# Kernel tuning notes

Measured on AMD Instinct MI355X. Metric: run time of the kernel, lower is better.

The kernel has to match this reference:

```python
import jax, jax.numpy as jnp
import numpy as np

WEIGHTS = {'seg': 1.0, 'grid': 0.5, 'baseline': 0.8, 'theta': 0.3, 'signal': 2.0}
IGNORE = 255


def _bce(p, t):
    # torch BCELoss: clamps log terms at -100
    lp = jnp.maximum(jnp.log(jnp.clip(p, 1e-12, 1.0)), -100.0)
    l1p = jnp.maximum(jnp.log(jnp.clip(1.0 - p, 1e-12, 1.0)), -100.0)
    return -(t * lp + (1.0 - t) * l1p).mean()


def _ce_ignore(logits, target):
    # logits (B,C,H,W), target (B,H,W) int; mean over target != 255
    logp = jax.nn.log_softmax(logits, axis=1)
    valid = target != IGNORE
    t_safe = jnp.where(valid, target, 0)
    nll = -jnp.take_along_axis(logp, t_safe[:, None].astype(jnp.int32), axis=1)[:, 0]
    return (nll * valid).sum() / jnp.maximum(valid.sum(), 1)


def _dice(logits, target, num_classes):
    p = jax.nn.softmax(logits, axis=1)                      # (B,C,H,W)
    oh = jax.nn.one_hot(target, num_classes, dtype=p.dtype) # (B,H,W,C)
    oh = jnp.transpose(oh, (0, 3, 1, 2))
    inter = (p * oh).sum(axis=(2, 3))
    union = p.sum(axis=(2, 3)) + oh.sum(axis=(2, 3))
    dice = (2.0 * inter + 1e-07) / (union + 1e-07)
    return 1.0 - dice.mean()


def _resize_bilinear_ac(x, out_h, out_w):
    # align_corners=True bilinear, x: (B,C,H,W)
    B, C, H, Wd = x.shape
    ys = jnp.linspace(0.0, H - 1.0, out_h)
    xs = jnp.linspace(0.0, Wd - 1.0, out_w)
    y0 = jnp.floor(ys).astype(jnp.int32); y1 = jnp.minimum(y0 + 1, H - 1); wy = (ys - y0).astype(x.dtype)
    x0 = jnp.floor(xs).astype(jnp.int32); x1 = jnp.minimum(x0 + 1, Wd - 1); wx = (xs - x0).astype(x.dtype)
    rows = x[:, :, y0, :] * (1 - wy)[None, None, :, None] + x[:, :, y1, :] * wy[None, None, :, None]
    out = rows[:, :, :, x0] * (1 - wx) + rows[:, :, :, x1] * wx
    return out


def _normalize_signal_masked(sig, mask):
    # sig, mask: (B,12,T); per-lead min/max normalize on valid region
    mf = mask.astype(sig.dtype)
    cnt = mf.sum(-1, keepdims=True)
    mn = jnp.min(jnp.where(mask, sig, jnp.inf), -1, keepdims=True)
    mx = jnp.max(jnp.where(mask, sig, -jnp.inf), -1, keepdims=True)
    rng = mx - mn
    ok = (cnt >= 2) & (rng >= 1e-06)
    mn_s = jnp.where(ok, mn, 0.0)
    rng_s = jnp.where(ok, rng, 1.0)
    norm = (2.0 * (sig - mn_s) / (rng_s + 1e-08) - 1.0) * mf
    return jnp.where(ok, norm, 0.0)


def _masked_mae(pred, target, mask):
    mf = mask.astype(pred.dtype)
    return (jnp.abs(pred - target) * mf).sum() / (mf.sum() + 1e-07)


def _masked_pearson(pred, target, mask):
    mf = mask.astype(pred.dtype)
    cnt = mf.sum(-1)                                   # (B,12)
    cs = jnp.maximum(cnt, 1.0)
    pm = (pred * mf).sum(-1) / cs
    tm = (target * mf).sum(-1) / cs
    pc = (pred - pm[..., None]) * mf
    tc = (target - tm[..., None]) * mf
    num = (pc * tc).sum(-1)
    ps = jnp.sqrt((pc ** 2).sum(-1) + 1e-06)
    ts = jnp.sqrt((tc ** 2).sum(-1) + 1e-06)
    corr = jnp.clip(num / (ps * ts + 1e-06), -1.0, 1.0)
    valid = (cnt >= 10).astype(pred.dtype)
    n_valid = valid.sum()
    avg = (corr * valid).sum() / jnp.maximum(n_valid, 1.0)
    return jnp.where(n_valid > 0, 1.0 - avg, 1.0)


def setup_inputs() -> dict:
    key = jax.random.key(0)
    ks = jax.random.split(key, 11)
    B, H, Wd, T = 8, 512, 512, 5000
    return {
        'wave_seg_pred': jax.random.normal(ks[0], (B, 13, H, Wd), jnp.float32),
        'wave_seg_target': jax.random.randint(ks[1], (B, H, Wd), 0, 13, jnp.int32),
        'grid_pred': jax.random.uniform(ks[2], (B, 1, H, Wd), jnp.float32),
        'grid_target': jax.random.uniform(ks[3], (B, 1, H, Wd), jnp.float32),
        'baseline_pred': jax.random.uniform(ks[4], (B, 12, H // 16, Wd // 16), jnp.float32),
        'baseline_target': jax.random.uniform(ks[5], (B, 12, H, Wd), jnp.float32),
        'theta_pred': jax.random.normal(ks[6], (B, 2, 3), jnp.float32),
        'theta_gt': jax.random.normal(ks[7], (B, 2, 3), jnp.float32),
        'signal_pred': jax.random.normal(ks[8], (B, 12, T), jnp.float32),
        'gt_signal': jax.random.normal(ks[9], (B, T, 12), jnp.float32),
        'signal_mask': jax.random.randint(ks[10], (B, T, 12), 0, 2, jnp.int32).astype(bool),
    }


def reference(wave_seg_pred, wave_seg_target, grid_pred, grid_target,
              baseline_pred, baseline_target, theta_pred, theta_gt,
              signal_pred, gt_signal, signal_mask):
    # seg
    seg = (_ce_ignore(wave_seg_pred, wave_seg_target)
           + _dice(wave_seg_pred, wave_seg_target, 13)) * WEIGHTS['seg']
    # grid
    inter = (grid_pred * grid_target).sum()
    union = grid_pred.sum() + grid_target.sum()
    grid = (_bce(grid_pred, grid_target)
            + (1.0 - (2.0 * inter + 1e-07) / (union + 1e-07))) * WEIGHTS['grid']
    # baseline
    Hp, Wp = baseline_pred.shape[2], baseline_pred.shape[3]
    bt = _resize_bilinear_ac(baseline_target, Hp, Wp)
    baseline = _bce(baseline_pred, bt) * WEIGHTS['baseline']
    # theta
    theta = jnp.abs(theta_pred - theta_gt).mean() * WEIGHTS['theta']
    # signal
    sig_t = jnp.swapaxes(gt_signal, 1, 2)     # (B,12,T)
    m = jnp.swapaxes(signal_mask, 1, 2)       # (B,12,T)
    pn = _normalize_signal_masked(signal_pred, m)
    tn = _normalize_signal_masked(sig_t, m)
    signal = (_masked_mae(pn, tn, m) + _masked_pearson(pn, tn, m)) * WEIGHTS['signal']
    total = seg + grid + baseline + theta + signal
    return jnp.stack([seg, grid, baseline, theta, signal, total])
```

## Files before the change

### kernel.cpp

```cpp
#include <hip/hip_runtime.h>
#include <math.h>

#define WS_SEG_NLL    0
#define WS_SEG_VALID  8
#define WS_INTER      16
#define WS_PSUM       120
#define WS_OHCNT      224
#define WS_GRID_BCE   328
#define WS_GRID_INTER 329
#define WS_GRID_PSUM  330
#define WS_GRID_TSUM  331
#define WS_BASE_BCE   332
#define WS_SIG_ABS    333
#define WS_SIG_CNT    334
#define WS_SIG_CORR   335
#define WS_SIG_NV     336
#define WS_FLOATS     338

__device__ inline float wave_sum(float v) {
    #pragma unroll
    for (int o = 32; o > 0; o >>= 1) v += __shfl_down(v, o, 64);
    return v;
}

template <int OP>
__device__ inline float blk_red(float v, float* sb) {
    #pragma unroll
    for (int o = 32; o > 0; o >>= 1) {
        float u = __shfl_down(v, o, 64);
        v = (OP == 0) ? (v + u) : ((OP == 1) ? fminf(v, u) : fmaxf(v, u));
    }
    __syncthreads();
    if ((threadIdx.x & 63) == 0) sb[threadIdx.x >> 6] = v;
    __syncthreads();
    const int nw = blockDim.x >> 6;
    float r = sb[0];
    for (int w = 1; w < nw; w++) {
        float u = sb[w];
        r = (OP == 0) ? (r + u) : ((OP == 1) ? fminf(r, u) : fmaxf(r, u));
    }
    return r;
}

__global__ __launch_bounds__(256) void seg_kernel(const float4* __restrict__ pred4,
                                                  const int4* __restrict__ tgt4,
                                                  float* __restrict__ ws) {
    const int b = blockIdx.y;
    const int HW  = 512 * 512;
    const int HW4 = HW / 4;
    const float4* predb = pred4 + (size_t)b * 13 * HW4;
    const int4* tgtb = tgt4 + (size_t)b * HW4;

    float psum[13], inter[13], cnt13[13];
    #pragma unroll
    for (int c = 0; c < 13; c++) { psum[c] = 0.f; inter[c] = 0.f; cnt13[c] = 0.f; }
    float nll = 0.f, nval = 0.f;

    const int stride = gridDim.x * blockDim.x;
    for (int i = blockIdx.x * blockDim.x + threadIdx.x; i < HW4; i += stride) {
        float4 x4[13];
        #pragma unroll
        for (int c = 0; c < 13; c++) x4[c] = predb[(size_t)c * HW4 + i];
        const int4 t4 = tgtb[i];
        const int ta[4] = {t4.x, t4.y, t4.z, t4.w};
        #pragma unroll
        for (int k = 0; k < 4; k++) {
            float x[13];
            #pragma unroll
            for (int c = 0; c < 13; c++)
                x[c] = (k == 0) ? x4[c].x : (k == 1) ? x4[c].y : (k == 2) ? x4[c].z : x4[c].w;
            const int t = ta[k];
            float m = x[0];
            #pragma unroll
            for (int c = 1; c < 13; c++) m = fmaxf(m, x[c]);
            float xt = x[0];
            #pragma unroll
            for (int c = 1; c < 13; c++) xt = (c == t) ? x[c] : xt;
            float se = 0.f;
            #pragma unroll
            for (int c = 0; c < 13; c++) { x[c] = __expf(x[c] - m); se += x[c]; }
            const float inv = 1.0f / se;
            #pragma unroll
            for (int c = 0; c < 13; c++) {
                const float p = x[c] * inv;
                psum[c] += p;
                const bool sel = (c == t);
                inter[c] += sel ? p : 0.f;
                cnt13[c] += sel ? 1.f : 0.f;
            }
            const bool valid = (t != 255);
            nll  += valid ? (m + __logf(se) - xt) : 0.f;
            nval += valid ? 1.f : 0.f;
        }
    }

    __shared__ float sred[41];
    if (threadIdx.x < 41) sred[threadIdx.x] = 0.f;
    __syncthreads();
    const bool lane0 = (threadIdx.x & 63) == 0;
    #pragma unroll
    for (int c = 0; c < 13; c++) {
        float a = wave_sum(psum[c]);  if (lane0) atomicAdd(&sred[c], a);
        float d = wave_sum(inter[c]); if (lane0) atomicAdd(&sred[13 + c], d);
        float e = wave_sum(cnt13[c]); if (lane0) atomicAdd(&sred[26 + c], e);
    }
    { float a = wave_sum(nll);  if (lane0) atomicAdd(&sred[39], a); }
    { float a = wave_sum(nval); if (lane0) atomicAdd(&sred[40], a); }
    __syncthreads();
    if (threadIdx.x < 13) {
        atomicAdd(&ws[WS_PSUM  + b * 13 + threadIdx.x], sred[threadIdx.x]);
        atomicAdd(&ws[WS_INTER + b * 13 + threadIdx.x], sred[13 + threadIdx.x]);
        atomicAdd(&ws[WS_OHCNT + b * 13 + threadIdx.x], sred[26 + threadIdx.x]);
    }
    if (threadIdx.x == 64) atomicAdd(&ws[WS_SEG_NLL + b],   sred[39]);
    if (threadIdx.x == 65) atomicAdd(&ws[WS_SEG_VALID + b], sred[40]);
}

__global__ __launch_bounds__(256) void grid_kernel(const float4* __restrict__ gp,
                                                   const float4* __restrict__ gt,
                                                   float* __restrict__ ws) {
    const int N4 = 2097152 / 4;
    float bce = 0.f, inter = 0.f, ps = 0.f, ts = 0.f;
    const int stride = gridDim.x * blockDim.x;
    for (int i = blockIdx.x * blockDim.x + threadIdx.x; i < N4; i += stride) {
        const float4 p4 = gp[i];
        const float4 t4 = gt[i];
        const float pa[4] = {p4.x, p4.y, p4.z, p4.w};
        const float ta[4] = {t4.x, t4.y, t4.z, t4.w};
        #pragma unroll
        for (int k = 0; k < 4; k++) {
            const float p = pa[k], t = ta[k];
            const float pc  = fminf(fmaxf(p, 1e-12f), 1.0f);
            const float qc  = fminf(fmaxf(1.f - p, 1e-12f), 1.0f);
            const float lp  = fmaxf(__logf(pc), -100.f);
            const float l1p = fmaxf(__logf(qc), -100.f);
            bce  -= t * lp + (1.f - t) * l1p;
            inter += p * t;
            ps += p;
            ts += t;
        }
    }
    __shared__ float s4[4];
    if (threadIdx.x < 4) s4[threadIdx.x] = 0.f;
    __syncthreads();
    const bool lane0 = (threadIdx.x & 63) == 0;
    { float a = wave_sum(bce);   if (lane0) atomicAdd(&s4[0], a); }
    { float a = wave_sum(inter); if (lane0) atomicAdd(&s4[1], a); }
    { float a = wave_sum(ps);    if (lane0) atomicAdd(&s4[2], a); }
    { float a = wave_sum(ts);    if (lane0) atomicAdd(&s4[3], a); }
    __syncthreads();
    if (threadIdx.x == 0) {
        atomicAdd(&ws[WS_GRID_BCE],   s4[0]);
        atomicAdd(&ws[WS_GRID_INTER], s4[1]);
        atomicAdd(&ws[WS_GRID_PSUM],  s4[2]);
        atomicAdd(&ws[WS_GRID_TSUM],  s4[3]);
    }
}

__global__ __launch_bounds__(256) void baseline_kernel(const float* __restrict__ bp,
                                                       const float* __restrict__ bt,
                                                       float* __restrict__ ws) {
    const int idx = blockIdx.x * blockDim.x + threadIdx.x;
    float bce = 0.f;
    {
        const int w  = idx & 31;
        const int h  = (idx >> 5) & 31;
        const int bc = idx >> 10;
        const float* img = bt + (size_t)bc * 262144;
        const float step = 511.0f / 31.0f;
        const float yy = h * step, xx = w * step;
        int y0 = (int)floorf(yy); int y1 = min(y0 + 1, 511); const float wy = yy - y0;
        int x0 = (int)floorf(xx); int x1 = min(x0 + 1, 511); const float wx = xx - x0;
        const float v00 = img[y0 * 512 + x0], v01 = img[y0 * 512 + x1];
        const float v10 = img[y1 * 512 + x0], v11 = img[y1 * 512 + x1];
        const float r0 = v00 * (1.f - wy) + v10 * wy;
        const float r1 = v01 * (1.f - wy) + v11 * wy;
        const float t  = r0 * (1.f - wx) + r1 * wx;
        const float p  = bp[idx];
        const float pc  = fminf(fmaxf(p, 1e-12f), 1.0f);
        const float qc  = fminf(fmaxf(1.f - p, 1e-12f), 1.0f);
        const float lp  = fmaxf(__logf(pc), -100.f);
        const float l1p = fmaxf(__logf(qc), -100.f);
        bce = -(t * lp + (1.f - t) * l1p);
    }
    __shared__ float sb[4];
    const float s = blk_red<0>(bce, sb);
    if (threadIdx.x == 0) atomicAdd(&ws[WS_BASE_BCE], s);
}

__global__ __launch_bounds__(256) void signal_kernel(const float* __restrict__ sp,
                                                     const float* __restrict__ st,
                                                     const void* __restrict__ mp,
                                                     float* __restrict__ ws) {
    const int T = 5000;
    const int bl = blockIdx.x;
    const int b = bl / 12, l = bl % 12;
    const float* ps = sp + (size_t)(b * 12 + l) * T;
    const float* ts_base = st + (size_t)b * T * 12 + l;
    const int* mi = (const int*)mp;
    const unsigned char* mb = (const unsigned char*)mp;
    const size_t mbase = (size_t)b * T * 12 + l;

    __shared__ float sb[4];
    __shared__ int s_flag;

    if (threadIdx.x == 0) s_flag = 0;
    __syncthreads();
    int f = 0;
    for (int i = threadIdx.x; i < 3072; i += blockDim.x)
        if ((i & 3) && mb[i]) f = 1;
    if (__any(f) && (threadIdx.x & 63) == 0) atomicOr(&s_flag, 1);
    __syncthreads();
    const bool m32 = (s_flag == 0);

    float cnt = 0.f;
    float mnp = __builtin_inff(), mxp = -__builtin_inff();
    float mnt = __builtin_inff(), mxt = -__builtin_inff();
    for (int t = threadIdx.x; t < T; t += blockDim.x) {
        const bool m = m32 ? (mi[mbase + (size_t)t * 12] != 0)
                           : (mb[mbase + (size_t)t * 12] != 0);
        const float p  = ps[t];
        const float tv = ts_base[(size_t)t * 12];
        if (m) {
            cnt += 1.f;
            mnp = fminf(mnp, p);  mxp = fmaxf(mxp, p);
            mnt = fminf(mnt, tv); mxt = fmaxf(mxt, tv);
        }
    }
    cnt = blk_red<0>(cnt, sb);
    mnp = blk_red<1>(mnp, sb); mxp = blk_red<2>(mxp, sb);
    mnt = blk_red<1>(mnt, sb); mxt = blk_red<2>(mxt, sb);

    const float rngp = mxp - mnp, rngt = mxt - mnt;
    const bool okp = (cnt >= 2.f) && (rngp >= 1e-6f);
    const bool okt = (cnt >= 2.f) && (rngt >= 1e-6f);
    const float mnp_s = okp ? mnp : 0.f, rp = okp ? rngp : 1.f;
    const float mnt_s = okt ? mnt : 0.f, rt = okt ? rngt : 1.f;
    const float invp = 2.f / (rp + 1e-8f), invt = 2.f / (rt + 1e-8f);

    float S_p = 0.f, S_t = 0.f, S_pt = 0.f, S_pp = 0.f, S_tt = 0.f, S_abs = 0.f;
    for (int t = threadIdx.x; t < T; t += blockDim.x) {
        const bool m = m32 ? (mi[mbase + (size_t)t * 12] != 0)
                           : (mb[mbase + (size_t)t * 12] != 0);
        const float p  = ps[t];
        const float tv = ts_base[(size_t)t * 12];
        const float pn = (m && okp) ? ((p  - mnp_s) * invp - 1.f) : 0.f;
        const float tn = (m && okt) ? ((tv - mnt_s) * invt - 1.f) : 0.f;
        S_p += pn; S_t += tn;
        S_pt += pn * tn; S_pp += pn * pn; S_tt += tn * tn;
        S_abs += m ? fabsf(pn - tn) : 0.f;
    }
    S_p  = blk_red<0>(S_p, sb);
    S_t  = blk_red<0>(S_t, sb);
    S_pt = blk_red<0>(S_pt, sb);
    S_pp = blk_red<0>(S_pp, sb);
    S_tt = blk_red<0>(S_tt, sb);
    S_abs = blk_red<0>(S_abs, sb);

    if (threadIdx.x == 0) {
        const float cs = fmaxf(cnt, 1.f);
        const float pm = S_p / cs, tm = S_t / cs;
        const float num = S_pt - pm * S_t - tm * S_p + pm * tm * cnt;
        const float psd = sqrtf(fmaxf(S_pp - 2.f * pm * S_p + pm * pm * cnt, 0.f) + 1e-6f);
        const float tsd = sqrtf(fmaxf(S_tt - 2.f * tm * S_t + tm * tm * cnt, 0.f) + 1e-6f);
        float corr = num / (psd * tsd + 1e-6f);
        corr = fminf(fmaxf(corr, -1.f), 1.f);
        const float valid = (cnt >= 10.f) ? 1.f : 0.f;
        atomicAdd(&ws[WS_SIG_ABS],  S_abs);
        atomicAdd(&ws[WS_SIG_CNT],  cnt);
        atomicAdd(&ws[WS_SIG_CORR], corr * valid);
        atomicAdd(&ws[WS_SIG_NV],   valid);
    }
}

__global__ __launch_bounds__(128) void finalize_kernel(const float* __restrict__ tp,
                                                       const float* __restrict__ tg,
                                                       const float* __restrict__ ws,
                                                       float* __restrict__ out) {
    __shared__ float s_d, s_nll, s_nv, s_th;
    if (threadIdx.x == 0) { s_d = 0.f; s_nll = 0.f; s_nv = 0.f; s_th = 0.f; }
    __syncthreads();
    const int t = threadIdx.x;
    float d = 0.f, nll = 0.f, nv = 0.f, th = 0.f;
    if (t < 104) {
        const float it = ws[WS_INTER + t], p = ws[WS_PSUM + t], oh = ws[WS_OHCNT + t];
        d = (2.f * it + 1e-7f) / (p + oh + 1e-7f);
    }
    if (t < 8) { nll = ws[WS_SEG_NLL + t]; nv = ws[WS_SEG_VALID + t]; }
    if (t < 48) th = fabsf(tp[t] - tg[t]);
    d = wave_sum(d); nll = wave_sum(nll); nv = wave_sum(nv); th = wave_sum(th);
    if ((t & 63) == 0) {
        atomicAdd(&s_d, d); atomicAdd(&s_nll, nll);
        atomicAdd(&s_nv, nv); atomicAdd(&s_th, th);
    }
    __syncthreads();
    if (t == 0) {
        const float ce = s_nll / fmaxf(s_nv, 1.f);
        const float seg = (ce + (1.f - s_d / 104.f)) * 1.0f;
        const float bce_g = ws[WS_GRID_BCE] / 2097152.f;
        const float gd = 1.f - (2.f * ws[WS_GRID_INTER] + 1e-7f) /
                               (ws[WS_GRID_PSUM] + ws[WS_GRID_TSUM] + 1e-7f);
        const float grid = (bce_g + gd) * 0.5f;
        const float base = (ws[WS_BASE_BCE] / 98304.f) * 0.8f;
        const float theta = (s_th / 48.f) * 0.3f;
        const float mae = ws[WS_SIG_ABS] / (ws[WS_SIG_CNT] + 1e-7f);
        const float nvs = ws[WS_SIG_NV];
        const float pear = (nvs > 0.f) ? (1.f - ws[WS_SIG_CORR] / fmaxf(nvs, 1.f)) : 1.f;
        const float sig = (mae + pear) * 2.0f;
        const float total = seg + grid + base + theta + sig;
        out[0] = seg; out[1] = grid; out[2] = base; out[3] = theta; out[4] = sig;
        out[5] = total;
    }
}

extern "C" void kernel_launch(void* const* d_in, const int* in_sizes, int n_in,
                              void* d_out, int out_size, void* d_ws, size_t ws_size,
                              hipStream_t stream) {
    const float* seg_pred  = (const float*)d_in[0];
    const int*   seg_tgt   = (const int*)d_in[1];
    const float* grid_pred = (const float*)d_in[2];
    const float* grid_tgt  = (const float*)d_in[3];
    const float* base_pred = (const float*)d_in[4];
    const float* base_tgt  = (const float*)d_in[5];
    const float* theta_p   = (const float*)d_in[6];
    const float* theta_g   = (const float*)d_in[7];
    const float* sig_p     = (const float*)d_in[8];
    const float* sig_t     = (const float*)d_in[9];
    const void*  maskp     = d_in[10];
    float* ws  = (float*)d_ws;
    float* out = (float*)d_out;

    hipMemsetAsync(d_ws, 0, WS_FLOATS * sizeof(float), stream);
    seg_kernel<<<dim3(128, 8), 256, 0, stream>>>((const float4*)seg_pred,
                                                 (const int4*)seg_tgt, ws);
    grid_kernel<<<128, 256, 0, stream>>>((const float4*)grid_pred, (const float4*)grid_tgt, ws);
    baseline_kernel<<<384, 256, 0, stream>>>(base_pred, base_tgt, ws);
    signal_kernel<<<96, 256, 0, stream>>>(sig_p, sig_t, maskp, ws);
    finalize_kernel<<<1, 128, 0, stream>>>(theta_p, theta_g, ws, out);
}
```

Baseline: 328.4 us.

## Merge loss kernels into one launch and split signal into two phases

Combines the seg, grid, baseline and signal-stats work into a single kernel dispatched by block index. The signal kernel is split into a stats phase and a second phase that also does the finalize step, using a last-block counter. Seg work is spread over many more blocks, with float2 loads, ballot-based counts and shared atomics for the intersection term. The intent is fewer launches and better occupancy on the large seg tensor, at the cost of more scattered shared atomics and an extra workspace round-trip for the signal statistics.

Result: faster. 304.8 us (-7.2%).

```diff
diff --git a/kernel.cpp b/kernel.cpp
--- a/kernel.cpp
+++ b/kernel.cpp
@@ -15,7 +15,16 @@
 #define WS_SIG_CNT    334
 #define WS_SIG_CORR   335
 #define WS_SIG_NV     336
-#define WS_FLOATS     338
+#define WS_MASK_FLAG  337
+#define WS_DONE       338
+#define WS_SIGSTATS   340
+#define WS_FLOATS     820
+
+#define SEG_NB   2048
+#define GRID_NB  256
+#define BASE_NB  384
+#define SIGA_NB  96
+#define TOTAL_NB (SEG_NB + GRID_NB + BASE_NB + SIGA_NB)
 
 __device__ inline float wave_sum(float v) {
     #pragma unroll
@@ -42,34 +51,46 @@
     return r;
 }
 
-__global__ __launch_bounds__(256) void seg_kernel(const float4* __restrict__ pred4,
-                                                  const int4* __restrict__ tgt4,
-                                                  float* __restrict__ ws) {
-    const int b = blockIdx.y;
-    const int HW  = 512 * 512;
-    const int HW4 = HW / 4;
-    const float4* predb = pred4 + (size_t)b * 13 * HW4;
-    const int4* tgtb = tgt4 + (size_t)b * HW4;
-
-    float psum[13], inter[13], cnt13[13];
-    #pragma unroll
-    for (int c = 0; c < 13; c++) { psum[c] = 0.f; inter[c] = 0.f; cnt13[c] = 0.f; }
-    float nll = 0.f, nval = 0.f;
-
-    const int stride = gridDim.x * blockDim.x;
-    for (int i = blockIdx.x * blockDim.x + threadIdx.x; i < HW4; i += stride) {
-        float4 x4[13];
+__device__ void seg_part(int sb_idx, const float2* __restrict__ pred2,
+                         const int2* __restrict__ tgt2, float* __restrict__ ws) {
+    const int b  = sb_idx >> 8;
+    const int xb = sb_idx & 255;
+    const int HW2 = 131072;
+    const float2* predb = pred2 + (size_t)b * 13 * HW2;
+    const int2*   tgtb  = tgt2 + (size_t)b * HW2;
+
+    __shared__ float s_inter[13];
+    __shared__ float s_psum[13];
+    __shared__ int   s_cnt[13];
+    __shared__ float s_nll;
+    __shared__ int   s_nval;
+    if (threadIdx.x < 13) { s_inter[threadIdx.x] = 0.f; s_psum[threadIdx.x] = 0.f; s_cnt[threadIdx.x] = 0; }
+    if (threadIdx.x == 13) s_nll = 0.f;
+    if (threadIdx.x == 14) s_nval = 0;
+    __syncthreads();
+
+    float psum[13];
+    #pragma unroll
+    for (int c = 0; c < 13; c++) psum[c] = 0.f;
+    int cnt[13];
+    #pragma unroll
+    for (int c = 0; c < 13; c++) cnt[c] = 0;
+    float nll = 0.f;
+    int nval = 0;
+
+    #pragma unroll
+    for (int it = 0; it < 2; it++) {
+        const int j = xb * 256 + threadIdx.x + it * 65536;
+        float2 x2[13];
         #pragma unroll
-        for (int c = 0; c < 13; c++) x4[c] = predb[(size_t)c * HW4 + i];
-        const int4 t4 = tgtb[i];
-        const int ta[4] = {t4.x, t4.y, t4.z, t4.w};
+        for (int c = 0; c < 13; c++) x2[c] = predb[c * HW2 + j];
+        const int2 t2 = tgtb[j];
         #pragma unroll
-        for (int k = 0; k < 4; k++) {
+        for (int k = 0; k < 2; k++) {
+            const int t = (k == 0) ? t2.x : t2.y;
             float x[13];
             #pragma unroll
-            for (int c = 0; c < 13; c++)
-                x[c] = (k == 0) ? x4[c].x : (k == 1) ? x4[c].y : (k == 2) ? x4[c].z : x4[c].w;
-            const int t = ta[k];
+            for (int c = 0; c < 13; c++) x[c] = (k == 0) ? x2[c].x : x2[c].y;
             float m = x[0];
             #pragma unroll
             for (int c = 1; c < 13; c++) m = fmaxf(m, x[c]);
@@ -79,50 +100,49 @@
             float se = 0.f;
             #pragma unroll
             for (int c = 0; c < 13; c++) { x[c] = __expf(x[c] - m); se += x[c]; }
-            const float inv = 1.0f / se;
-            #pragma unroll
-            for (int c = 0; c < 13; c++) {
-                const float p = x[c] * inv;
-                psum[c] += p;
-                const bool sel = (c == t);
-                inter[c] += sel ? p : 0.f;
-                cnt13[c] += sel ? 1.f : 0.f;
+            const float inv = __builtin_amdgcn_rcpf(se);
+            #pragma unroll
+            for (int c = 0; c < 13; c++) psum[c] += x[c] * inv;
+            #pragma unroll
+            for (int c = 0; c < 13; c++) cnt[c] += __popcll(__ballot(t == c));
+            nval += __popcll(__ballot(t != 255));
+            const bool valid = (t != 255);
+            if ((unsigned)t < 13u) {
+                const float pt = __expf(xt - m) * inv;
+                atomicAdd(&s_inter[t], pt);
             }
-            const bool valid = (t != 255);
-            nll  += valid ? (m + __logf(se) - xt) : 0.f;
-            nval += valid ? 1.f : 0.f;
+            nll += valid ? (m + __logf(se) - xt) : 0.f;
         }
     }
 
-    __shared__ float sred[41];
-    if (threadIdx.x < 41) sred[threadIdx.x] = 0.f;
-    __syncthreads();
     const bool lane0 = (threadIdx.x & 63) == 0;
     #pragma unroll
     for (int c = 0; c < 13; c++) {
-        float a = wave_sum(psum[c]);  if (lane0) atomicAdd(&sred[c], a);
-        float d = wave_sum(inter[c]); if (lane0) atomicAdd(&sred[13 + c], d);
-        float e = wave_sum(cnt13[c]); if (lane0) atomicAdd(&sred[26 + c], e);
-    }
-    { float a = wave_sum(nll);  if (lane0) atomicAdd(&sred[39], a); }
-    { float a = wave_sum(nval); if (lane0) atomicAdd(&sred[40], a); }
+        float a = wave_sum(psum[c]);
+        if (lane0) atomicAdd(&s_psum[c], a);
+    }
+    { float a = wave_sum(nll); if (lane0) atomicAdd(&s_nll, a); }
+    if (lane0) {
+        #pragma unroll
+        for (int c = 0; c < 13; c++) atomicAdd(&s_cnt[c], cnt[c]);
+        atomicAdd(&s_nval, nval);
+    }
     __syncthreads();
     if (threadIdx.x < 13) {
-        atomicAdd(&ws[WS_PSUM  + b * 13 + threadIdx.x], sred[threadIdx.x]);
-        atomicAdd(&ws[WS_INTER + b * 13 + threadIdx.x], sred[13 + threadIdx.x]);
-        atomicAdd(&ws[WS_OHCNT + b * 13 + threadIdx.x], sred[26 + threadIdx.x]);
-    }
-    if (threadIdx.x == 64) atomicAdd(&ws[WS_SEG_NLL + b],   sred[39]);
-    if (threadIdx.x == 65) atomicAdd(&ws[WS_SEG_VALID + b], sred[40]);
-}
-
-__global__ __launch_bounds__(256) void grid_kernel(const float4* __restrict__ gp,
-                                                   const float4* __restrict__ gt,
-                                                   float* __restrict__ ws) {
+        atomicAdd(&ws[WS_PSUM  + b * 13 + threadIdx.x], s_psum[threadIdx.x]);
+        atomicAdd(&ws[WS_INTER + b * 13 + threadIdx.x], s_inter[threadIdx.x]);
+        atomicAdd(&ws[WS_OHCNT + b * 13 + threadIdx.x], (float)s_cnt[threadIdx.x]);
+    }
+    if (threadIdx.x == 64) atomicAdd(&ws[WS_SEG_NLL + b],   s_nll);
+    if (threadIdx.x == 65) atomicAdd(&ws[WS_SEG_VALID + b], (float)s_nval);
+}
+
+__device__ void grid_part(int gb, const float4* __restrict__ gp,
+                          const float4* __restrict__ gt, float* __restrict__ ws) {
     const int N4 = 2097152 / 4;
     float bce = 0.f, inter = 0.f, ps = 0.f, ts = 0.f;
-    const int stride = gridDim.x * blockDim.x;
-    for (int i = blockIdx.x * blockDim.x + threadIdx.x; i < N4; i += stride) {
+    const int stride = GRID_NB * 256;
+    for (int i = gb * 256 + threadIdx.x; i < N4; i += stride) {
         const float4 p4 = gp[i];
         const float4 t4 = gt[i];
         const float pa[4] = {p4.x, p4.y, p4.z, p4.w};
@@ -157,44 +177,39 @@
     }
 }
 
-__global__ __launch_bounds__(256) void baseline_kernel(const float* __restrict__ bp,
-                                                       const float* __restrict__ bt,
-                                                       float* __restrict__ ws) {
-    const int idx = blockIdx.x * blockDim.x + threadIdx.x;
-    float bce = 0.f;
-    {
-        const int w  = idx & 31;
-        const int h  = (idx >> 5) & 31;
-        const int bc = idx >> 10;
-        const float* img = bt + (size_t)bc * 262144;
-        const float step = 511.0f / 31.0f;
-        const float yy = h * step, xx = w * step;
-        int y0 = (int)floorf(yy); int y1 = min(y0 + 1, 511); const float wy = yy - y0;
-        int x0 = (int)floorf(xx); int x1 = min(x0 + 1, 511); const float wx = xx - x0;
-        const float v00 = img[y0 * 512 + x0], v01 = img[y0 * 512 + x1];
-        const float v10 = img[y1 * 512 + x0], v11 = img[y1 * 512 + x1];
-        const float r0 = v00 * (1.f - wy) + v10 * wy;
-        const float r1 = v01 * (1.f - wy) + v11 * wy;
-        const float t  = r0 * (1.f - wx) + r1 * wx;
-        const float p  = bp[idx];
-        const float pc  = fminf(fmaxf(p, 1e-12f), 1.0f);
-        const float qc  = fminf(fmaxf(1.f - p, 1e-12f), 1.0f);
-        const float lp  = fmaxf(__logf(pc), -100.f);
-        const float l1p = fmaxf(__logf(qc), -100.f);
-        bce = -(t * lp + (1.f - t) * l1p);
-    }
+__device__ void base_part(int bb, const float* __restrict__ bp,
+                          const float* __restrict__ bt, float* __restrict__ ws) {
+    const int idx = bb * 256 + threadIdx.x;
+    const int w  = idx & 31;
+    const int h  = (idx >> 5) & 31;
+    const int bc = idx >> 10;
+    const float* img = bt + (size_t)bc * 262144;
+    const float step = 511.0f / 31.0f;
+    const float yy = h * step, xx = w * step;
+    int y0 = (int)floorf(yy); int y1 = min(y0 + 1, 511); const float wy = yy - y0;
+    int x0 = (int)floorf(xx); int x1 = min(x0 + 1, 511); const float wx = xx - x0;
+    const float v00 = img[y0 * 512 + x0], v01 = img[y0 * 512 + x1];
+    const float v10 = img[y1 * 512 + x0], v11 = img[y1 * 512 + x1];
+    const float r0 = v00 * (1.f - wy) + v10 * wy;
+    const float r1 = v01 * (1.f - wy) + v11 * wy;
+    const float t  = r0 * (1.f - wx) + r1 * wx;
+    const float p  = bp[idx];
+    const float pc  = fminf(fmaxf(p, 1e-12f), 1.0f);
+    const float qc  = fminf(fmaxf(1.f - p, 1e-12f), 1.0f);
+    const float lp  = fmaxf(__logf(pc), -100.f);
+    const float l1p = fmaxf(__logf(qc), -100.f);
+    const float bce = -(t * lp + (1.f - t) * l1p);
+
     __shared__ float sb[4];
     const float s = blk_red<0>(bce, sb);
     if (threadIdx.x == 0) atomicAdd(&ws[WS_BASE_BCE], s);
 }
 
-__global__ __launch_bounds__(256) void signal_kernel(const float* __restrict__ sp,
-                                                     const float* __restrict__ st,
-                                                     const void* __restrict__ mp,
-                                                     float* __restrict__ ws) {
+__device__ void sigA_part(int sl, const float* __restrict__ sp,
+                          const float* __restrict__ st, const void* __restrict__ mp,
+                          float* __restrict__ ws) {
     const int T = 5000;
-    const int bl = blockIdx.x;
-    const int b = bl / 12, l = bl % 12;
+    const int b = sl / 12, l = sl % 12;
     const float* ps = sp + (size_t)(b * 12 + l) * T;
     const float* ts_base = st + (size_t)b * T * 12 + l;
     const int* mi = (const int*)mp;
@@ -203,7 +218,6 @@
 
     __shared__ float sb[4];
     __shared__ int s_flag;
-
     if (threadIdx.x == 0) s_flag = 0;
     __syncthreads();
     int f = 0;
@@ -231,6 +245,51 @@
     mnp = blk_red<1>(mnp, sb); mxp = blk_red<2>(mxp, sb);
     mnt = blk_red<1>(mnt, sb); mxt = blk_red<2>(mxt, sb);
 
+    if (threadIdx.x == 0) {
+        float* o = ws + WS_SIGSTATS + sl * 5;
+        o[0] = cnt; o[1] = mnp; o[2] = mxp; o[3] = mnt; o[4] = mxt;
+        if (sl == 0) ws[WS_MASK_FLAG] = m32 ? 1.0f : 0.0f;
+    }
+}
+
+__global__ __launch_bounds__(256) void mega_kernel(
+        const float2* __restrict__ seg_pred, const int2* __restrict__ seg_tgt,
+        const float4* __restrict__ grid_pred, const float4* __restrict__ grid_tgt,
+        const float* __restrict__ base_pred, const float* __restrict__ base_tgt,
+        const float* __restrict__ sig_p, const float* __restrict__ sig_t,
+        const void* __restrict__ maskp, float* __restrict__ ws) {
+    const int bx = blockIdx.x;
+    if (bx < SEG_NB) {
+        seg_part(bx, seg_pred, seg_tgt, ws);
+    } else if (bx < SEG_NB + GRID_NB) {
+        grid_part(bx - SEG_NB, grid_pred, grid_tgt, ws);
+    } else if (bx < SEG_NB + GRID_NB + BASE_NB) {
+        base_part(bx - SEG_NB - GRID_NB, base_pred, base_tgt, ws);
+    } else {
+        sigA_part(bx - SEG_NB - GRID_NB - BASE_NB, sig_p, sig_t, maskp, ws);
+    }
+}
+
+__global__ __launch_bounds__(256) void sigB_kernel(
+        const float* __restrict__ sp, const float* __restrict__ st,
+        const void* __restrict__ mp, const float* __restrict__ tp,
+        const float* __restrict__ tg, float* __restrict__ ws,
+        float* __restrict__ out) {
+    const int T = 5000;
+    const int sl = blockIdx.x;
+    const int b = sl / 12, l = sl % 12;
+    const float* ps = sp + (size_t)(b * 12 + l) * T;
+    const float* ts_base = st + (size_t)b * T * 12 + l;
+    const int* mi = (const int*)mp;
+    const unsigned char* mb = (const unsigned char*)mp;
+    const size_t mbase = (size_t)b * T * 12 + l;
+
+    __shared__ float sb[4];
+    const bool m32 = ws[WS_MASK_FLAG] > 0.5f;
+    const float* stats = ws + WS_SIGSTATS + sl * 5;
+    const float cnt = stats[0];
+    const float mnp = stats[1], mxp = stats[2], mnt = stats[3], mxt = stats[4];
+
     const float rngp = mxp - mnp, rngt = mxt - mnt;
     const bool okp = (cnt >= 2.f) && (rngp >= 1e-6f);
     const bool okt = (cnt >= 2.f) && (rngt >= 1e-6f);
@@ -257,6 +316,7 @@
     S_tt = blk_red<0>(S_tt, sb);
     S_abs = blk_red<0>(S_abs, sb);
 
+    __shared__ int s_last;
     if (threadIdx.x == 0) {
         const float cs = fmaxf(cnt, 1.f);
         const float pm = S_p / cs, tm = S_t / cs;
@@ -270,13 +330,13 @@
         atomicAdd(&ws[WS_SIG_CNT],  cnt);
         atomicAdd(&ws[WS_SIG_CORR], corr * valid);
         atomicAdd(&ws[WS_SIG_NV],   valid);
-    }
-}
-
-__global__ __launch_bounds__(128) void finalize_kernel(const float* __restrict__ tp,
-                                                       const float* __restrict__ tg,
-                                                       const float* __restrict__ ws,
-                                                       float* __restrict__ out) {
+        __threadfence();
+        const int old = atomicAdd((int*)(ws + WS_DONE), 1);
+        s_last = (old == 95) ? 1 : 0;
+    }
+    __syncthreads();
+    if (!s_last) return;
+
     __shared__ float s_d, s_nll, s_nv, s_th;
     if (threadIdx.x == 0) { s_d = 0.f; s_nll = 0.f; s_nv = 0.f; s_th = 0.f; }
     __syncthreads();
@@ -303,9 +363,12 @@
         const float grid = (bce_g + gd) * 0.5f;
         const float base = (ws[WS_BASE_BCE] / 98304.f) * 0.8f;
         const float theta = (s_th / 48.f) * 0.3f;
-        const float mae = ws[WS_SIG_ABS] / (ws[WS_SIG_CNT] + 1e-7f);
-        const float nvs = ws[WS_SIG_NV];
-        const float pear = (nvs > 0.f) ? (1.f - ws[WS_SIG_CORR] / fmaxf(nvs, 1.f)) : 1.f;
+        const float sabs = atomicAdd(&ws[WS_SIG_ABS],  0.f);
+        const float scnt = atomicAdd(&ws[WS_SIG_CNT],  0.f);
+        const float scor = atomicAdd(&ws[WS_SIG_CORR], 0.f);
+        const float snv  = atomicAdd(&ws[WS_SIG_NV],   0.f);
+        const float mae = sabs / (scnt + 1e-7f);
+        const float pear = (snv > 0.f) ? (1.f - scor / fmaxf(snv, 1.f)) : 1.f;
         const float sig = (mae + pear) * 2.0f;
         const float total = seg + grid + base + theta + sig;
         out[0] = seg; out[1] = grid; out[2] = base; out[3] = theta; out[4] = sig;
@@ -331,10 +394,9 @@
     float* out = (float*)d_out;
 
     hipMemsetAsync(d_ws, 0, WS_FLOATS * sizeof(float), stream);
-    seg_kernel<<<dim3(128, 8), 256, 0, stream>>>((const float4*)seg_pred,
-                                                 (const int4*)seg_tgt, ws);
-    grid_kernel<<<128, 256, 0, stream>>>((const float4*)grid_pred, (const float4*)grid_tgt, ws);
-    baseline_kernel<<<384, 256, 0, stream>>>(base_pred, base_tgt, ws);
-    signal_kernel<<<96, 256, 0, stream>>>(sig_p, sig_t, maskp, ws);
-    finalize_kernel<<<1, 128, 0, stream>>>(theta_p, theta_g, ws, out);
-}
+    mega_kernel<<<TOTAL_NB, 256, 0, stream>>>(
+        (const float2*)seg_pred, (const int2*)seg_tgt,
+        (const float4*)grid_pred, (const float4*)grid_tgt,
+        base_pred, base_tgt, sig_p, sig_t, maskp, ws);
+    sigB_kernel<<<96, 256, 0, stream>>>(sig_p, sig_t, maskp, theta_p, theta_g, ws, out);
+}
```
